# Kernel optimization log

Hardware: AMD Instinct MI355X
Metric: run time of the kernel (lower is better)

## Reference

```python
import jax, jax.numpy as jnp
import numpy as np
from jax.ops import segment_sum

N_NODES = 50000


def gcn_conv(x, W, b, src, dst, n_nodes):
    """Standard PyG GCNConv: self-loops + symmetric deg^-1/2 normalization."""
    h = x @ W  # [N, H]
    loop = jnp.arange(n_nodes, dtype=src.dtype)
    s = jnp.concatenate([src, loop])
    d = jnp.concatenate([dst, loop])
    deg = segment_sum(jnp.ones_like(d, dtype=h.dtype), d, num_segments=n_nodes)
    dinv = jnp.where(deg > 0, jax.lax.rsqrt(deg), 0.0)
    norm = dinv[s] * dinv[d]  # [E+N]
    msg = h[s] * norm[:, None]  # gather + scale
    out = segment_sum(msg, d, num_segments=n_nodes)  # scatter-add
    return out + b


def setup_inputs() -> dict:
    key = jax.random.key(0)
    ks = jax.random.split(key, 12)
    node_in, hidden = 256, 128
    n_edges = 1_600_000
    x = jax.random.normal(ks[0], (N_NODES, node_in), dtype=jnp.float32)
    edge_index = jax.random.randint(ks[1], (2, n_edges), 0, N_NODES, dtype=jnp.int64)

    def glorot(k, fan_in, fan_out):
        lim = np.sqrt(6.0 / (fan_in + fan_out)).astype(np.float32)
        return jax.random.uniform(k, (fan_in, fan_out), jnp.float32, -lim, lim)

    W1 = glorot(ks[2], node_in, hidden)
    b1 = jnp.zeros((hidden,), jnp.float32)
    W2 = glorot(ks[3], hidden, hidden)
    b2 = jnp.zeros((hidden,), jnp.float32)
    W3 = glorot(ks[4], 2 * hidden, hidden)
    b3 = jnp.zeros((hidden,), jnp.float32)
    W4 = glorot(ks[5], hidden, 1)
    b4 = jnp.zeros((1,), jnp.float32)
    return {"x": x, "edge_index": edge_index, "W1": W1, "b1": b1,
            "W2": W2, "b2": b2, "W3": W3, "b3": b3, "W4": W4, "b4": b4}


def reference(x, edge_index, W1, b1, W2, b2, W3, b3, W4, b4):
    src, dst = edge_index[0], edge_index[1]
    h = gcn_conv(x, W1, b1, src, dst, N_NODES)
    h = jax.nn.relu(h)  # dropout is identity in eval mode
    h = gcn_conv(h, W2, b2, src, dst, N_NODES)
    # gather node pairs per edge, concat, MLP edge classifier
    ef = jnp.concatenate([h[src], h[dst]], axis=1)  # [E, 2H]
    z = jax.nn.relu(ef @ W3 + b3)
    scores = jax.nn.sigmoid(z @ W4 + b4)
    return scores.squeeze(-1)
```

## Files before the change

### kernel.cpp

```cpp
#include <hip/hip_runtime.h>
#include <math.h>

typedef unsigned short ushort_t;
typedef __attribute__((ext_vector_type(8))) short bf16x8;
typedef __attribute__((ext_vector_type(8))) unsigned short us8;
typedef __attribute__((ext_vector_type(4))) float f32x4;

__device__ __forceinline__ float bf2f(unsigned short u) {
    union { unsigned int i; float f; } x; x.i = ((unsigned int)u) << 16; return x.f;
}
__device__ __forceinline__ unsigned short f2bf(float f) {
    union { float f; unsigned int i; } x; x.f = f;
    unsigned int lsb = (x.i >> 16) & 1u;
    return (unsigned short)((x.i + 0x7fffu + lsb) >> 16);
}


__global__ __launch_bounds__(1024) void detect_i64(const int* __restrict__ ei,
                                                   int nwords, int* __restrict__ flag) {
    __shared__ int s_any;
    if (threadIdx.x == 0) s_any = 0;
    __syncthreads();
    int any = 0;
    for (int i = threadIdx.x; 2 * i + 1 < nwords; i += 1024)
        if (ei[2 * i + 1] != 0) any = 1;
    if (any) s_any = 1;
    __syncthreads();
    if (threadIdx.x == 0) flag[0] = (s_any == 0) ? 1 : 0;
}

__global__ __launch_bounds__(256) void normalize_idx(const int* __restrict__ ei, int E,
                                                     const int* __restrict__ flag,
                                                     int* __restrict__ s_out,
                                                     int* __restrict__ d_out) {
    int e = blockIdx.x * 256 + threadIdx.x;
    if (e >= E) return;
    if (flag[0]) {
        s_out[e] = ei[2 * e];
        d_out[e] = ei[2 * (E + e)];
    } else {
        s_out[e] = ei[e];
        d_out[e] = ei[E + e];
    }
}


__global__ __launch_bounds__(256) void zero_i32(int* __restrict__ p, int n) {
    int i = blockIdx.x * 256 + threadIdx.x;
    if (i < n) p[i] = 0;
}

__global__ __launch_bounds__(256) void count_deg_part(const int* __restrict__ dst,
                                                      int* __restrict__ deg,
                                                      int E, int RB) {
    int xcd = blockIdx.x & 7;
    int e = (blockIdx.x >> 3) * 256 + threadIdx.x;
    if (e >= E) return;
    int d = dst[e];
    if ((unsigned)(d - xcd * RB) < (unsigned)RB) atomicAdd(&deg[d], 1);
}

__global__ __launch_bounds__(1024) void scan_kernel(const int* __restrict__ deg,
                                                    int* __restrict__ offs,
                                                    int* __restrict__ cursor,
                                                    float* __restrict__ dinv, int n) {
    __shared__ int wsum[16];
    __shared__ int s_carry;
    int tid = threadIdx.x, lane = tid & 63, wid = tid >> 6;
    if (tid == 0) s_carry = 0;
    __syncthreads();
    for (int base = 0; base < n; base += 1024) {
        int i = base + tid;
        int v = (i < n) ? deg[i] : 0;
        int x = v;
        #pragma unroll
        for (int d = 1; d < 64; d <<= 1) {
            int y = __shfl_up(x, d, 64);
            if (lane >= d) x += y;
        }
        if (lane == 63) wsum[wid] = x;
        __syncthreads();
        int carry = s_carry;
        __syncthreads();
        if (tid == 0) {
            int run = 0;
            #pragma unroll
            for (int w = 0; w < 16; ++w) { int t = wsum[w]; wsum[w] = run; run += t; }
            s_carry = carry + run;
        }
        __syncthreads();
        if (i < n) {
            int excl = carry + wsum[wid] + (x - v);
            offs[i] = excl;
            cursor[i] = excl;
            dinv[i] = rsqrtf((float)(v + 1));
        }
        __syncthreads();
    }
    if (tid == 0) offs[n] = s_carry;
}

__global__ __launch_bounds__(256) void fill_csr_part(const int* __restrict__ src,
                                                     const int* __restrict__ dst,
                                                     int* __restrict__ cursor,
                                                     int2* __restrict__ csr_se,
                                                     int E, int RB) {
    int xcd = blockIdx.x & 7;
    int e = (blockIdx.x >> 3) * 256 + threadIdx.x;
    if (e >= E) return;
    int d = dst[e];
    if ((unsigned)(d - xcd * RB) < (unsigned)RB) {
        int pos = atomicAdd(&cursor[d], 1);
        csr_se[pos] = make_int2(src[e], e);
    }
}


__global__ __launch_bounds__(256) void conv_weights(const float* __restrict__ W1,
                                                    const float* __restrict__ W2,
                                                    const float* __restrict__ W3,
                                                    ushort_t* __restrict__ Wt1,
                                                    ushort_t* __restrict__ Wt2,
                                                    ushort_t* __restrict__ Wt3a,
                                                    ushort_t* __restrict__ Wt3b) {
    int t = blockIdx.x * 256 + threadIdx.x;
    if (t < 32768) {
        int k = t >> 7, n = t & 127;
        Wt1[n * 256 + k] = f2bf(W1[t]);
    } else if (t < 49152) {
        int u = t - 32768; int k = u >> 7, n = u & 127;
        Wt2[n * 128 + k] = f2bf(W2[u]);
    } else if (t < 65536) {
        int u = t - 49152; int k = u >> 7, n = u & 127;
        Wt3a[n * 128 + k] = f2bf(W3[u]);
    } else if (t < 81920) {
        int u = t - 65536; int k = u >> 7, n = u & 127;
        Wt3b[n * 128 + k] = f2bf(W3[128 * 128 + u]);
    }
}


#define ASTR 40
#define BSTR 136

__global__ __launch_bounds__(256) void gemm_mfma(const float* __restrict__ A,
                                                 const ushort_t* __restrict__ Wt,
                                                 ushort_t* __restrict__ outp,
                                                 const float* __restrict__ dinv,
                                                 const float* __restrict__ bias,
                                                 int M, int K) {
    __shared__ __attribute__((aligned(16))) ushort_t Bt[128 * BSTR];
    __shared__ __attribute__((aligned(16))) ushort_t As[64 * ASTR];
    int tid = threadIdx.x;
    int wave = tid >> 6, lane = tid & 63;
    int l15 = lane & 15, lg = lane >> 4;
    int block_m = blockIdx.x * 64;
    f32x4 acc[8];
    #pragma unroll
    for (int i = 0; i < 8; ++i) acc[i] = (f32x4){0.f, 0.f, 0.f, 0.f};

    for (int kh = 0; kh < K; kh += 128) {
        #pragma unroll
        for (int i = 0; i < 16; ++i) {
            int u = i * 256 + tid;
            int col = u >> 5;
            int kq = (u & 31) * 4;
            ushort4 w = *(const ushort4*)(&Wt[(size_t)col * K + kh + kq]);
            *(ushort4*)(&Bt[col * BSTR + kq]) = w;
        }
        for (int k0 = kh; k0 < kh + 128; k0 += 32) {
            #pragma unroll
            for (int rep = 0; rep < 2; ++rep) {
                int unit = rep * 256 + tid;
                int r = unit >> 3;
                int kc = (unit & 7) * 4;
                int gr = block_m + r;
                int grc = gr < M ? gr : M - 1;
                float4 v = *(const float4*)(&A[(size_t)grc * K + k0 + kc]);
                if (gr >= M) v = make_float4(0.f, 0.f, 0.f, 0.f);
                ushort4 p;
                p.x = f2bf(v.x); p.y = f2bf(v.y); p.z = f2bf(v.z); p.w = f2bf(v.w);
                *(ushort4*)(&As[r * ASTR + kc]) = p;
            }
            __syncthreads();
            bf16x8 af = *(const bf16x8*)(&As[(wave * 16 + l15) * ASTR + lg * 8]);
            #pragma unroll
            for (int nf = 0; nf < 8; ++nf) {
                bf16x8 bf = *(const bf16x8*)(&Bt[(nf * 16 + l15) * BSTR +
                                                 (k0 - kh) + lg * 8]);
                acc[nf] = __builtin_amdgcn_mfma_f32_16x16x32_bf16(af, bf, acc[nf],
                                                                  0, 0, 0);
            }
            __syncthreads();
        }
    }
    int orow = block_m + wave * 16 + lg * 4;
    #pragma unroll
    for (int nf = 0; nf < 8; ++nf) {
        int col = nf * 16 + l15;
        float bb = bias ? bias[col] : 0.f;
        #pragma unroll
        for (int j = 0; j < 4; ++j) {
            int m = orow + j;
            if (m < M) {
                float s = dinv ? dinv[m] : 1.f;
                outp[(size_t)m * 128 + col] = f2bf(acc[nf][j] * s + bb);
            }
        }
    }
}


__global__ __launch_bounds__(256) void gemm_regB(const ushort_t* __restrict__ A,
                                                 const ushort_t* __restrict__ Wt,
                                                 ushort_t* __restrict__ outp,
                                                 const float* __restrict__ dinv,
                                                 const float* __restrict__ bias,
                                                 int M) {
    int tid = threadIdx.x;
    int wave = tid >> 6, lane = tid & 63;
    int l15 = lane & 15, lg = lane >> 4;
    bf16x8 Bf[8][4];
    #pragma unroll
    for (int nf = 0; nf < 8; ++nf)
        #pragma unroll
        for (int ks = 0; ks < 4; ++ks)
            Bf[nf][ks] = *(const bf16x8*)(&Wt[(size_t)(nf * 16 + l15) * 128 +
                                              ks * 32 + lg * 8]);
    float bv[8];
    #pragma unroll
    for (int nf = 0; nf < 8; ++nf)
        bv[nf] = bias ? bias[nf * 16 + l15] : 0.f;

    int nt = (M + 15) >> 4;
    for (int tile = blockIdx.x * 4 + wave; tile < nt; tile += gridDim.x * 4) {
        int r = tile * 16 + l15;
        const ushort_t* Ar = A + (size_t)(r < M ? r : M - 1) * 128;
        bf16x8 af0 = *(const bf16x8*)(Ar + 0 * 32 + lg * 8);
        bf16x8 af1 = *(const bf16x8*)(Ar + 1 * 32 + lg * 8);
        bf16x8 af2 = *(const bf16x8*)(Ar + 2 * 32 + lg * 8);
        bf16x8 af3 = *(const bf16x8*)(Ar + 3 * 32 + lg * 8);
        f32x4 acc[8];
        #pragma unroll
        for (int i = 0; i < 8; ++i) acc[i] = (f32x4){0.f, 0.f, 0.f, 0.f};
        #pragma unroll
        for (int nf = 0; nf < 8; ++nf) {
            acc[nf] = __builtin_amdgcn_mfma_f32_16x16x32_bf16(af0, Bf[nf][0], acc[nf], 0, 0, 0);
            acc[nf] = __builtin_amdgcn_mfma_f32_16x16x32_bf16(af1, Bf[nf][1], acc[nf], 0, 0, 0);
            acc[nf] = __builtin_amdgcn_mfma_f32_16x16x32_bf16(af2, Bf[nf][2], acc[nf], 0, 0, 0);
            acc[nf] = __builtin_amdgcn_mfma_f32_16x16x32_bf16(af3, Bf[nf][3], acc[nf], 0, 0, 0);
        }
        int orow = tile * 16 + lg * 4;
        #pragma unroll
        for (int nf = 0; nf < 8; ++nf) {
            int col = nf * 16 + l15;
            #pragma unroll
            for (int j = 0; j < 4; ++j) {
                int m = orow + j;
                if (m < M) {
                    float s = dinv ? dinv[m] : 1.f;
                    outp[(size_t)m * 128 + col] = f2bf(acc[nf][j] * s + bv[nf]);
                }
            }
        }
    }
}


__global__ __launch_bounds__(256) void pull_agg(const ushort_t* __restrict__ g,
                                                const int2* __restrict__ csr_se,
                                                const int* __restrict__ offs,
                                                const float* __restrict__ dinv,
                                                const float* __restrict__ bias,
                                                ushort_t* __restrict__ out,
                                                int n_nodes, int do_relu) {
    int tid = threadIdx.x;
    int wid = tid >> 6, lane = tid & 63;
    int q = lane >> 4, c = lane & 15;
    int node = blockIdx.x * 4 + wid;
    if (node >= n_nodes) return;
    int beg = offs[node], end = offs[node + 1];
    float acc[8] = {};
    int i = beg;
    for (; i + 8 <= end; i += 8) {
        int s1 = csr_se[i + q].x;
        int s2 = csr_se[i + 4 + q].x;
        us8 r1 = *(const us8*)(g + (size_t)s1 * 128 + c * 8);
        us8 r2 = *(const us8*)(g + (size_t)s2 * 128 + c * 8);
        acc[0] += bf2f(r1[0]); acc[1] += bf2f(r1[1]);
        acc[2] += bf2f(r1[2]); acc[3] += bf2f(r1[3]);
        acc[4] += bf2f(r1[4]); acc[5] += bf2f(r1[5]);
        acc[6] += bf2f(r1[6]); acc[7] += bf2f(r1[7]);
        acc[0] += bf2f(r2[0]); acc[1] += bf2f(r2[1]);
        acc[2] += bf2f(r2[2]); acc[3] += bf2f(r2[3]);
        acc[4] += bf2f(r2[4]); acc[5] += bf2f(r2[5]);
        acc[6] += bf2f(r2[6]); acc[7] += bf2f(r2[7]);
    }
    for (; i < end; i += 4) {
        int j = i + q;
        int sidx = (j < end) ? csr_se[j].x : n_nodes;
        us8 r = *(const us8*)(g + (size_t)sidx * 128 + c * 8);
        acc[0] += bf2f(r[0]); acc[1] += bf2f(r[1]);
        acc[2] += bf2f(r[2]); acc[3] += bf2f(r[3]);
        acc[4] += bf2f(r[4]); acc[5] += bf2f(r[5]);
        acc[6] += bf2f(r[6]); acc[7] += bf2f(r[7]);
    }
    #pragma unroll
    for (int k = 0; k < 8; ++k) {
        acc[k] += __shfl_xor(acc[k], 16, 64);
        acc[k] += __shfl_xor(acc[k], 32, 64);
    }
    us8 sr = *(const us8*)(g + (size_t)node * 128 + c * 8);
    float s = dinv[node];
    float4 ba = *(const float4*)(&bias[c * 8]);
    float4 bb = *(const float4*)(&bias[c * 8 + 4]);
    float o[8];
    o[0] = (acc[0] + bf2f(sr[0])) * s + ba.x;
    o[1] = (acc[1] + bf2f(sr[1])) * s + ba.y;
    o[2] = (acc[2] + bf2f(sr[2])) * s + ba.z;
    o[3] = (acc[3] + bf2f(sr[3])) * s + ba.w;
    o[4] = (acc[4] + bf2f(sr[4])) * s + bb.x;
    o[5] = (acc[5] + bf2f(sr[5])) * s + bb.y;
    o[6] = (acc[6] + bf2f(sr[6])) * s + bb.z;
    o[7] = (acc[7] + bf2f(sr[7])) * s + bb.w;
    if (do_relu) {
        #pragma unroll
        for (int k = 0; k < 8; ++k) o[k] = fmaxf(o[k], 0.f);
    }
    if (q == 0) {
        us8 w;
        #pragma unroll
        for (int k = 0; k < 8; ++k) w[k] = f2bf(o[k]);
        *(us8*)(out + (size_t)node * 128 + c * 8) = w;
    }
}


__device__ __forceinline__ float edot8(const us8& uu, const float* vr,
                                       const float4& wa, const float4& wb) {
    float ps;
    ps  = fmaxf(bf2f(uu[0]) + vr[0], 0.f) * wa.x;
    ps += fmaxf(bf2f(uu[1]) + vr[1], 0.f) * wa.y;
    ps += fmaxf(bf2f(uu[2]) + vr[2], 0.f) * wa.z;
    ps += fmaxf(bf2f(uu[3]) + vr[3], 0.f) * wa.w;
    ps += fmaxf(bf2f(uu[4]) + vr[4], 0.f) * wb.x;
    ps += fmaxf(bf2f(uu[5]) + vr[5], 0.f) * wb.y;
    ps += fmaxf(bf2f(uu[6]) + vr[6], 0.f) * wb.z;
    ps += fmaxf(bf2f(uu[7]) + vr[7], 0.f) * wb.w;
    ps += __shfl_xor(ps, 8, 64);
    ps += __shfl_xor(ps, 4, 64);
    ps += __shfl_xor(ps, 2, 64);
    ps += __shfl_xor(ps, 1, 64);
    return ps;
}

__global__ __launch_bounds__(256) void edge_score_seg(const ushort_t* __restrict__ u,
                                                      const ushort_t* __restrict__ v,
                                                      const int2* __restrict__ csr_se,
                                                      const int* __restrict__ offs,
                                                      const float* __restrict__ W4,
                                                      const float* __restrict__ b4,
                                                      float* __restrict__ out,
                                                      int n_nodes) {
    int tid = threadIdx.x;
    int grp = tid >> 4, c = tid & 15;
    int node = blockIdx.x * 16 + grp;
    if (node >= n_nodes) return;
    int beg = offs[node], end = offs[node + 1];
    if (beg == end) return;
    us8 vv = *(const us8*)(v + (size_t)node * 128 + c * 8);
    float vr[8];
    #pragma unroll
    for (int k = 0; k < 8; ++k) vr[k] = bf2f(vv[k]);
    float4 wa = *(const float4*)(&W4[c * 8]);
    float4 wb = *(const float4*)(&W4[c * 8 + 4]);
    float b4v = b4[0];
    int p = beg;
    for (; p + 4 <= end; p += 4) {
        int2 se0 = csr_se[p];
        int2 se1 = csr_se[p + 1];
        int2 se2 = csr_se[p + 2];
        int2 se3 = csr_se[p + 3];
        us8 u0 = *(const us8*)(u + (size_t)se0.x * 128 + c * 8);
        us8 u1 = *(const us8*)(u + (size_t)se1.x * 128 + c * 8);
        us8 u2 = *(const us8*)(u + (size_t)se2.x * 128 + c * 8);
        us8 u3 = *(const us8*)(u + (size_t)se3.x * 128 + c * 8);
        float p0 = edot8(u0, vr, wa, wb);
        float p1 = edot8(u1, vr, wa, wb);
        float p2 = edot8(u2, vr, wa, wb);
        float p3 = edot8(u3, vr, wa, wb);
        if (c == 0) {
            out[se0.y] = 1.f / (1.f + expf(-(p0 + b4v)));
            out[se1.y] = 1.f / (1.f + expf(-(p1 + b4v)));
            out[se2.y] = 1.f / (1.f + expf(-(p2 + b4v)));
            out[se3.y] = 1.f / (1.f + expf(-(p3 + b4v)));
        }
    }
    for (; p < end; ++p) {
        int2 se = csr_se[p];
        us8 uu = *(const us8*)(u + (size_t)se.x * 128 + c * 8);
        float ps = edot8(uu, vr, wa, wb);
        if (c == 0)
            out[se.y] = 1.f / (1.f + expf(-(ps + b4v)));
    }
}


extern "C" void kernel_launch(void* const* d_in, const int* in_sizes, int n_in,
                              void* d_out, int out_size, void* d_ws, size_t ws_size,
                              hipStream_t stream) {
    const float* x  = (const float*)d_in[0];
    const int*   ei = (const int*)d_in[1];
    const float* W1 = (const float*)d_in[2];
    const float* b1 = (const float*)d_in[3];
    const float* W2 = (const float*)d_in[4];
    const float* b2 = (const float*)d_in[5];
    const float* W3 = (const float*)d_in[6];
    const float* b3 = (const float*)d_in[7];
    const float* W4 = (const float*)d_in[8];
    const float* b4 = (const float*)d_in[9];

    int N = in_sizes[0] / 256;
    int E = in_sizes[1] / 2;

    char* ws = (char*)d_ws;
    size_t off = 0;
    auto alloc = [&](size_t bytes) -> void* {
        void* p = ws + off;
        off += (bytes + 255) & ~(size_t)255;
        return p;
    };
    int*      flag    = (int*)     alloc(256);
    int*      srcn    = (int*)     alloc((size_t)E * 4);
    int*      dstn    = (int*)     alloc((size_t)E * 4);
    int*      deg     = (int*)     alloc((size_t)N * 4);
    int*      offs    = (int*)     alloc((size_t)(N + 1) * 4);
    int*      cursor  = (int*)     alloc((size_t)N * 4);
    float*    dinv    = (float*)   alloc((size_t)N * 4);
    int2*     csr_se  = (int2*)    alloc((size_t)E * 8);
    ushort_t* gbuf    = (ushort_t*)alloc((size_t)(N + 1) * 128 * 2);
    ushort_t* ubuf    = (ushort_t*)alloc((size_t)N * 128 * 2);
    ushort_t* vbuf    = (ushort_t*)alloc((size_t)N * 128 * 2);
    ushort_t* hbuf    = (ushort_t*)alloc((size_t)N * 128 * 2);
    ushort_t* Wt1     = (ushort_t*)alloc(128 * 256 * 2);
    ushort_t* Wt2     = (ushort_t*)alloc(128 * 128 * 2);
    ushort_t* Wt3a    = (ushort_t*)alloc(128 * 128 * 2);
    ushort_t* Wt3b    = (ushort_t*)alloc(128 * 128 * 2);
    (void)ws_size; (void)n_in; (void)out_size;

    float* outp = (float*)d_out;
    int gE = (E + 255) / 256;
    int gN4 = (N + 3) / 4;
    int RB = (N + 7) / 8;

    int nwords = (2 * E < 4096) ? 2 * E : 4096;
    detect_i64<<<1, 1024, 0, stream>>>(ei, nwords, flag);
    normalize_idx<<<gE, 256, 0, stream>>>(ei, E, flag, srcn, dstn);
    conv_weights<<<320, 256, 0, stream>>>(W1, W2, W3, Wt1, Wt2, Wt3a, Wt3b);

    zero_i32<<<(N + 255) / 256, 256, 0, stream>>>(deg, N);
    zero_i32<<<1, 256, 0, stream>>>((int*)(gbuf + (size_t)N * 128), 64);
    count_deg_part<<<gE * 8, 256, 0, stream>>>(dstn, deg, E, RB);
    scan_kernel<<<1, 1024, 0, stream>>>(deg, offs, cursor, dinv, N);
    fill_csr_part<<<gE * 8, 256, 0, stream>>>(srcn, dstn, cursor, csr_se, E, RB);

    int gM = (N + 63) / 64;
    gemm_mfma<<<gM, 256, 0, stream>>>(x, Wt1, gbuf, dinv, nullptr, N, 256);
    pull_agg<<<gN4, 256, 0, stream>>>(gbuf, csr_se, offs, dinv, b1, hbuf, N, 1);
    gemm_regB<<<512, 256, 0, stream>>>(hbuf, Wt2, gbuf, dinv, nullptr, N);
    pull_agg<<<gN4, 256, 0, stream>>>(gbuf, csr_se, offs, dinv, b2, hbuf, N, 0);
    gemm_regB<<<512, 256, 0, stream>>>(hbuf, Wt3a, ubuf, nullptr, nullptr, N);
    gemm_regB<<<512, 256, 0, stream>>>(hbuf, Wt3b, vbuf, nullptr, b3, N);
    edge_score_seg<<<(N + 15) / 16, 256, 0, stream>>>(ubuf, vbuf, csr_se, offs,
                                                      W4, b4, outp, N);
}
```

Measured before the change: 580.0 us.

## Parallelize degree scan across blocks and deepen unrolling in aggregation and edge scoring

Replaces the single-block serial degree prefix scan with a three-kernel multi-block scan (per-block scan, top-level scan of block sums, finalize). It also unrolls the pull aggregation loop to 16 edges per iteration and the edge scoring loop to 8 edges per iteration, so more gather loads are in flight. The scan costs two extra launches and an extra buffer, but removes a long serial loop run by one workgroup. The wider unrolls raise register pressure. The multi-block scan supports at most 256 blocks, which is enough for the 50000 nodes here.

```diff
diff --git a/kernel.cpp b/kernel.cpp
--- a/kernel.cpp
+++ b/kernel.cpp
@@ -60,44 +60,68 @@
     if ((unsigned)(d - xcd * RB) < (unsigned)RB) atomicAdd(&deg[d], 1);
 }
 
-__global__ __launch_bounds__(1024) void scan_kernel(const int* __restrict__ deg,
-                                                    int* __restrict__ offs,
-                                                    int* __restrict__ cursor,
-                                                    float* __restrict__ dinv, int n) {
-    __shared__ int wsum[16];
-    __shared__ int s_carry;
+__global__ __launch_bounds__(256) void scan_blk(const int* __restrict__ deg,
+                                                int* __restrict__ excl,
+                                                int* __restrict__ bsum, int n) {
+    __shared__ int wsum[4];
+    int i = blockIdx.x * 256 + threadIdx.x;
+    int lane = threadIdx.x & 63, wid = threadIdx.x >> 6;
+    int v = (i < n) ? deg[i] : 0;
+    int x = v;
+    #pragma unroll
+    for (int d = 1; d < 64; d <<= 1) {
+        int y = __shfl_up(x, d, 64);
+        if (lane >= d) x += y;
+    }
+    if (lane == 63) wsum[wid] = x;
+    __syncthreads();
+    if (threadIdx.x == 0) {
+        int run = 0;
+        #pragma unroll
+        for (int w = 0; w < 4; ++w) { int t = wsum[w]; wsum[w] = run; run += t; }
+        bsum[blockIdx.x] = run;
+    }
+    __syncthreads();
+    if (i < n) excl[i] = wsum[wid] + (x - v);
+}
+
+__global__ __launch_bounds__(256) void scan_top(int* __restrict__ bsum, int nb) {
+    __shared__ int wsum[4];
     int tid = threadIdx.x, lane = tid & 63, wid = tid >> 6;
-    if (tid == 0) s_carry = 0;
+    int v = (tid < nb) ? bsum[tid] : 0;
+    int x = v;
+    #pragma unroll
+    for (int d = 1; d < 64; d <<= 1) {
+        int y = __shfl_up(x, d, 64);
+        if (lane >= d) x += y;
+    }
+    if (lane == 63) wsum[wid] = x;
     __syncthreads();
-    for (int base = 0; base < n; base += 1024) {
-        int i = base + tid;
-        int v = (i < n) ? deg[i] : 0;
-        int x = v;
-        #pragma unroll
-        for (int d = 1; d < 64; d <<= 1) {
-            int y = __shfl_up(x, d, 64);
-            if (lane >= d) x += y;
-        }
-        if (lane == 63) wsum[wid] = x;
-        __syncthreads();
-        int carry = s_carry;
-        __syncthreads();
-        if (tid == 0) {
-            int run = 0;
-            #pragma unroll
-            for (int w = 0; w < 16; ++w) { int t = wsum[w]; wsum[w] = run; run += t; }
-            s_carry = carry + run;
-        }
-        __syncthreads();
-        if (i < n) {
-            int excl = carry + wsum[wid] + (x - v);
-            offs[i] = excl;
-            cursor[i] = excl;
-            dinv[i] = rsqrtf((float)(v + 1));
-        }
-        __syncthreads();
-    }
-    if (tid == 0) offs[n] = s_carry;
+    if (tid == 0) {
+        int run = 0;
+        #pragma unroll
+        for (int w = 0; w < 4; ++w) { int t = wsum[w]; wsum[w] = run; run += t; }
+        bsum[nb] = run;
+    }
+    __syncthreads();
+    if (tid < nb) bsum[tid] = wsum[wid] + (x - v);
+}
+
+__global__ __launch_bounds__(256) void scan_fin(const int* __restrict__ deg,
+                                                const int* __restrict__ excl,
+                                                const int* __restrict__ bsum,
+                                                int* __restrict__ offs,
+                                                int* __restrict__ cursor,
+                                                float* __restrict__ dinv,
+                                                int n, int nb) {
+    int i = blockIdx.x * 256 + threadIdx.x;
+    if (i < n) {
+        int e = excl[i] + bsum[blockIdx.x];
+        offs[i] = e;
+        cursor[i] = e;
+        dinv[i] = rsqrtf((float)(deg[i] + 1));
+    }
+    if (i == 0) offs[n] = bsum[nb];
 }
 
 __global__ __launch_bounds__(256) void fill_csr_part(const int* __restrict__ src,
@@ -267,6 +291,13 @@
 }
 
 
+__device__ __forceinline__ void acc8(float* acc, const us8& r) {
+    acc[0] += bf2f(r[0]); acc[1] += bf2f(r[1]);
+    acc[2] += bf2f(r[2]); acc[3] += bf2f(r[3]);
+    acc[4] += bf2f(r[4]); acc[5] += bf2f(r[5]);
+    acc[6] += bf2f(r[6]); acc[7] += bf2f(r[7]);
+}
+
 __global__ __launch_bounds__(256) void pull_agg(const ushort_t* __restrict__ g,
                                                 const int2* __restrict__ csr_se,
                                                 const int* __restrict__ offs,
@@ -282,28 +313,22 @@
     int beg = offs[node], end = offs[node + 1];
     float acc[8] = {};
     int i = beg;
-    for (; i + 8 <= end; i += 8) {
-        int s1 = csr_se[i + q].x;
-        int s2 = csr_se[i + 4 + q].x;
-        us8 r1 = *(const us8*)(g + (size_t)s1 * 128 + c * 8);
-        us8 r2 = *(const us8*)(g + (size_t)s2 * 128 + c * 8);
-        acc[0] += bf2f(r1[0]); acc[1] += bf2f(r1[1]);
-        acc[2] += bf2f(r1[2]); acc[3] += bf2f(r1[3]);
-        acc[4] += bf2f(r1[4]); acc[5] += bf2f(r1[5]);
-        acc[6] += bf2f(r1[6]); acc[7] += bf2f(r1[7]);
-        acc[0] += bf2f(r2[0]); acc[1] += bf2f(r2[1]);
-        acc[2] += bf2f(r2[2]); acc[3] += bf2f(r2[3]);
-        acc[4] += bf2f(r2[4]); acc[5] += bf2f(r2[5]);
-        acc[6] += bf2f(r2[6]); acc[7] += bf2f(r2[7]);
+    for (; i + 16 <= end; i += 16) {
+        int sA = csr_se[i + q].x;
+        int sB = csr_se[i + 4 + q].x;
+        int sC = csr_se[i + 8 + q].x;
+        int sD = csr_se[i + 12 + q].x;
+        us8 rA = *(const us8*)(g + (size_t)sA * 128 + c * 8);
+        us8 rB = *(const us8*)(g + (size_t)sB * 128 + c * 8);
+        us8 rC = *(const us8*)(g + (size_t)sC * 128 + c * 8);
+        us8 rD = *(const us8*)(g + (size_t)sD * 128 + c * 8);
+        acc8(acc, rA); acc8(acc, rB); acc8(acc, rC); acc8(acc, rD);
     }
     for (; i < end; i += 4) {
         int j = i + q;
         int sidx = (j < end) ? csr_se[j].x : n_nodes;
         us8 r = *(const us8*)(g + (size_t)sidx * 128 + c * 8);
-        acc[0] += bf2f(r[0]); acc[1] += bf2f(r[1]);
-        acc[2] += bf2f(r[2]); acc[3] += bf2f(r[3]);
-        acc[4] += bf2f(r[4]); acc[5] += bf2f(r[5]);
-        acc[6] += bf2f(r[6]); acc[7] += bf2f(r[7]);
+        acc8(acc, r);
     }
     #pragma unroll
     for (int k = 0; k < 8; ++k) {
@@ -376,11 +401,41 @@
     float4 wb = *(const float4*)(&W4[c * 8 + 4]);
     float b4v = b4[0];
     int p = beg;
+    for (; p + 8 <= end; p += 8) {
+        int2 se0 = csr_se[p];     int2 se1 = csr_se[p + 1];
+        int2 se2 = csr_se[p + 2]; int2 se3 = csr_se[p + 3];
+        int2 se4 = csr_se[p + 4]; int2 se5 = csr_se[p + 5];
+        int2 se6 = csr_se[p + 6]; int2 se7 = csr_se[p + 7];
+        us8 u0 = *(const us8*)(u + (size_t)se0.x * 128 + c * 8);
+        us8 u1 = *(const us8*)(u + (size_t)se1.x * 128 + c * 8);
+        us8 u2 = *(const us8*)(u + (size_t)se2.x * 128 + c * 8);
+        us8 u3 = *(const us8*)(u + (size_t)se3.x * 128 + c * 8);
+        us8 u4 = *(const us8*)(u + (size_t)se4.x * 128 + c * 8);
+        us8 u5 = *(const us8*)(u + (size_t)se5.x * 128 + c * 8);
+        us8 u6 = *(const us8*)(u + (size_t)se6.x * 128 + c * 8);
+        us8 u7 = *(const us8*)(u + (size_t)se7.x * 128 + c * 8);
+        float p0 = edot8(u0, vr, wa, wb);
+        float p1 = edot8(u1, vr, wa, wb);
+        float p2 = edot8(u2, vr, wa, wb);
+        float p3 = edot8(u3, vr, wa, wb);
+        float p4 = edot8(u4, vr, wa, wb);
+        float p5 = edot8(u5, vr, wa, wb);
+        float p6 = edot8(u6, vr, wa, wb);
+        float p7 = edot8(u7, vr, wa, wb);
+        if (c == 0) {
+            out[se0.y] = 1.f / (1.f + expf(-(p0 + b4v)));
+            out[se1.y] = 1.f / (1.f + expf(-(p1 + b4v)));
+            out[se2.y] = 1.f / (1.f + expf(-(p2 + b4v)));
+            out[se3.y] = 1.f / (1.f + expf(-(p3 + b4v)));
+            out[se4.y] = 1.f / (1.f + expf(-(p4 + b4v)));
+            out[se5.y] = 1.f / (1.f + expf(-(p5 + b4v)));
+            out[se6.y] = 1.f / (1.f + expf(-(p6 + b4v)));
+            out[se7.y] = 1.f / (1.f + expf(-(p7 + b4v)));
+        }
+    }
     for (; p + 4 <= end; p += 4) {
-        int2 se0 = csr_se[p];
-        int2 se1 = csr_se[p + 1];
-        int2 se2 = csr_se[p + 2];
-        int2 se3 = csr_se[p + 3];
+        int2 se0 = csr_se[p];     int2 se1 = csr_se[p + 1];
+        int2 se2 = csr_se[p + 2]; int2 se3 = csr_se[p + 3];
         us8 u0 = *(const us8*)(u + (size_t)se0.x * 128 + c * 8);
         us8 u1 = *(const us8*)(u + (size_t)se1.x * 128 + c * 8);
         us8 u2 = *(const us8*)(u + (size_t)se2.x * 128 + c * 8);
@@ -436,6 +491,8 @@
     int*      deg     = (int*)     alloc((size_t)N * 4);
     int*      offs    = (int*)     alloc((size_t)(N + 1) * 4);
     int*      cursor  = (int*)     alloc((size_t)N * 4);
+    int*      excl    = (int*)     alloc((size_t)N * 4);
+    int*      bsum    = (int*)     alloc(1024);
     float*    dinv    = (float*)   alloc((size_t)N * 4);
     int2*     csr_se  = (int2*)    alloc((size_t)E * 8);
     ushort_t* gbuf    = (ushort_t*)alloc((size_t)(N + 1) * 128 * 2);
@@ -451,6 +508,7 @@
     float* outp = (float*)d_out;
     int gE = (E + 255) / 256;
     int gN4 = (N + 3) / 4;
+    int nb = (N + 255) / 256;
     int RB = (N + 7) / 8;
 
     int nwords = (2 * E < 4096) ? 2 * E : 4096;
@@ -461,7 +519,9 @@
     zero_i32<<<(N + 255) / 256, 256, 0, stream>>>(deg, N);
     zero_i32<<<1, 256, 0, stream>>>((int*)(gbuf + (size_t)N * 128), 64);
     count_deg_part<<<gE * 8, 256, 0, stream>>>(dstn, deg, E, RB);
-    scan_kernel<<<1, 1024, 0, stream>>>(deg, offs, cursor, dinv, N);
+    scan_blk<<<nb, 256, 0, stream>>>(deg, excl, bsum, N);
+    scan_top<<<1, 256, 0, stream>>>(bsum, nb);
+    scan_fin<<<nb, 256, 0, stream>>>(deg, excl, bsum, offs, cursor, dinv, N, nb);
     fill_csr_part<<<gE * 8, 256, 0, stream>>>(srcn, dstn, cursor, csr_se, E, RB);
 
     int gM = (N + 63) / 64;
```

Result: faster. 531.1 us (-8.4%).
